# Performance work log

Measured on AMD Instinct MI355X. Metric: run time of the kernel, lower is better.

## Reference

```python
import jax, jax.numpy as jnp
import numpy as np

NEG_SLOPE = 0.15
MASK_VAL = -1e9


def setup_inputs() -> dict:
    key = jax.random.key(0)
    k1, k2, k3, k4, k5 = jax.random.split(key, 5)
    B, N, D, H, QKV = 4, 1024, 128, 8, 16
    h = jax.random.normal(k1, (B, N, D), dtype=jnp.float32)
    same_cluster = jax.random.randint(k2, (B, N, N), 0, 2) > 0
    # nn.Linear weights stored as [in, out] (x @ W); scaled like default init
    Wa = jax.random.normal(k3, (2 * D + 1, H), dtype=jnp.float32) / np.sqrt(2 * D + 1)
    Wv = jax.random.normal(k4, (D, H * QKV), dtype=jnp.float32) / np.sqrt(D)
    Wo = jax.random.normal(k5, (H * QKV, D), dtype=jnp.float32) / np.sqrt(H * QKV)
    return {"h": h, "same_cluster": same_cluster, "Wa": Wa, "Wv": Wv, "Wo": Wo, "local_only": 0}


def reference(h, same_cluster, Wa, Wv, Wo, local_only):
    B, N, D = h.shape
    H = Wa.shape[1]
    # concat([hi, hj, edge]) @ Wa == hi @ Wa[:D] + hj @ Wa[D:2D] + edge * Wa[2D]
    Wa_i, Wa_j, w_e = Wa[:D], Wa[D:2 * D], Wa[2 * D]  # [D,H], [D,H], [H]
    s_i = h @ Wa_i  # [B, N, H]
    s_j = h @ Wa_j  # [B, N, H]
    edge = same_cluster.astype(h.dtype)  # [B, N, N]
    scores = s_i[:, :, None, :] + s_j[:, None, :, :] + edge[..., None] * w_e  # [B,N,N,H]
    scores = jax.nn.leaky_relu(scores, negative_slope=NEG_SLOPE)
    scores = jnp.moveaxis(scores, -1, 1)  # [B, H, N, N]
    if local_only:
        scores = jnp.where(same_cluster[:, None, :, :], scores, MASK_VAL)
    alpha = jax.nn.softmax(scores, axis=-1)  # [B, H, N, N]
    v = (h @ Wv).reshape(B, N, H, -1).transpose(0, 2, 1, 3)  # [B, H, N, qkv]
    out = jnp.einsum('bhij,bhjd->bhid', alpha, v)  # [B, H, N, qkv]
    out = out.transpose(0, 2, 1, 3).reshape(B, N, -1)  # [B, N, H*qkv]
    return out @ Wo  # [B, N, D]
```

## Files before the change

### kernel.cpp

```cpp
#include <hip/hip_runtime.h>
#include <hip/hip_fp16.h>


#define NEG_SLOPE 0.15f
#define LOG2E 1.442695040888963f
#define B_ 4
#define N_ 1024
#define D_ 128
#define H_ 8
#define QKV_ 16
#define BN_ (B_ * N_)

typedef _Float16 half8 __attribute__((ext_vector_type(8)));
typedef float f32x4 __attribute__((ext_vector_type(4)));

#define WS_BYTES ((size_t)3932160)

__global__ __launch_bounds__(256) void prep_kernel(
    const float* __restrict__ h, const int* __restrict__ edge,
    const float* __restrict__ Wa, const float* __restrict__ Wv,
    float* __restrict__ SIt, float* __restrict__ SJt,
    _Float16* __restrict__ VT, unsigned long long* __restrict__ EM)
{
    __shared__ float hl[8][128];
    const int t  = threadIdx.x;
    const int w  = t >> 6;
    const int l  = t & 63;
    const int R0 = blockIdx.x * 8;

    {
        const int f = t * 4;
        *(float4*)(&hl[0][0] + f) = *(const float4*)(h + (size_t)R0 * 128 + f);
    }
    __syncthreads();

    const int cq = t & 31, rq = t >> 5;
    const int c4 = cq * 4;
    float a0 = 0.f, a1 = 0.f, a2 = 0.f, a3 = 0.f;
    #pragma unroll 8
    for (int k = 0; k < 128; ++k) {
        const float4 wv = *(const float4*)(Wv + k * 128 + c4);
        const float a = hl[rq][k];
        a0 += a * wv.x; a1 += a * wv.y; a2 += a * wv.z; a3 += a * wv.w;
    }
    {
        const int R = R0 + rq, b = R >> 10, n = R & 1023;
        const int head = cq >> 2, dd = (cq & 3) * 4;
        _Float16* vt = VT + ((size_t)(b * H_ + head) * 16 + dd) * N_ + n;
        vt[0]      = (_Float16)a0;
        vt[N_]     = (_Float16)a1;
        vt[2 * N_] = (_Float16)a2;
        vt[3 * N_] = (_Float16)a3;
    }

    {
        const int task = t >> 1, half = t & 1;
        const int row = task >> 4, which = (task >> 3) & 1, hh = task & 7;
        const float* wcol = Wa + which * 128 * H_ + hh;
        float s = 0.f;
        #pragma unroll 8
        for (int kk = 0; kk < 64; ++kk) {
            const int k = half * 64 + kk;
            s += hl[row][k] * wcol[k * H_];
        }
        s += __shfl_xor(s, 1, 64);
        if (!half) (which ? SJt : SIt)[hh * BN_ + R0 + row] = s * LOG2E;
    }

    #pragma unroll
    for (int rr = 0; rr < 2; ++rr) {
        const int R = R0 + w * 2 + rr;
        const int* erow = edge + (size_t)R * N_;
        #pragma unroll 4
        for (int s = 0; s < 16; ++s) {
            const unsigned long long mk = __ballot(erow[s * 64 + l] != 0);
            if (l == 0) EM[(size_t)R * 16 + s] = mk;
        }
    }
}

__global__ __launch_bounds__(256) void attn_kernel(
    const float* __restrict__ SIt, const float* __restrict__ SJt,
    const _Float16* __restrict__ VT, const unsigned long long* __restrict__ EM,
    const float* __restrict__ Wa, const int* __restrict__ local_only,
    float* __restrict__ ATT)
{
    const int t  = threadIdx.x;
    const int w  = t >> 6;
    const int l  = t & 63;
    const int m  = l & 15;
    const int kq = l >> 4;
    const int hh = blockIdx.y;
    const int b  = blockIdx.z;
    const int i0 = blockIdx.x * 16;
    const int bn0 = b * N_;

    const float we = Wa[2 * D_ * H_ + hh] * LOG2E;
    const int   lo = local_only[0];

    const float sim   = SIt[hh * BN_ + bn0 + i0 + m];
    const float simwe = sim + we;
    const float simNE = lo ? -1e6f : sim;

    const float*         sjrow = SJt + hh * BN_ + bn0;
    const _Float16*      vrow  = VT + ((size_t)(b * H_ + hh) * 16 + m) * N_;
    const unsigned char* EMb   = (const unsigned char*)EM;
    const size_t         eb0   = (size_t)(bn0 + i0 + m) * 128 + w * 32 + kq;

    f32x4 acc = {0.f, 0.f, 0.f, 0.f};
    float dsum = 0.f;

    const int wj0 = w * 256;
    #pragma unroll 2
    for (int c = 0; c < 8; ++c) {
        const int jb = wj0 + c * 32 + kq * 8;
        const float4 sjA = *(const float4*)(sjrow + jb);
        const float4 sjB = *(const float4*)(sjrow + jb + 4);
        const half8  bf  = *(const half8*)(vrow + jb);
        const int    eb  = EMb[eb0 + c * 4];

        const float sj[8] = {sjA.x, sjA.y, sjA.z, sjA.w,
                             sjB.x, sjB.y, sjB.z, sjB.w};
        half8 av;
        #pragma unroll
        for (int u = 0; u < 8; ++u) {
            const float x  = (((eb >> u) & 1) ? simwe : simNE) + sj[u];
            const float sc = fmaxf(x, NEG_SLOPE * x);
            const float p  = exp2f(sc);
            dsum += p;
            av[u] = (_Float16)p;
        }
        acc = __builtin_amdgcn_mfma_f32_16x16x32_f16(av, bf, acc, 0, 0, 0);
    }

    dsum += __shfl_xor(dsum, 16, 64);
    dsum += __shfl_xor(dsum, 32, 64);

    __shared__ float olds[4][16][17];
    __shared__ float denl[4][16];
    #pragma unroll
    for (int reg = 0; reg < 4; ++reg)
        olds[w][kq * 4 + reg][m] = acc[reg];
    if (l < 16) denl[w][l] = dsum;
    __syncthreads();

    {
        const int i = t >> 4, d = t & 15;
        const float o   = olds[0][i][d] + olds[1][i][d]
                        + olds[2][i][d] + olds[3][i][d];
        const float den = denl[0][i] + denl[1][i] + denl[2][i] + denl[3][i];
        ATT[(size_t)(bn0 + i0 + i) * 128 + hh * 16 + d] = o / den;
    }
}

__global__ __launch_bounds__(256) void out_kernel(
    const float* __restrict__ ATT, const float* __restrict__ Wo,
    float* __restrict__ out)
{
    __shared__ float al[8][128];
    const int t  = threadIdx.x;
    const int R0 = blockIdx.x * 8;
    {
        const int f = t * 4;
        *(float4*)(&al[0][0] + f) = *(const float4*)(ATT + (size_t)R0 * 128 + f);
    }
    __syncthreads();

    const int cq = t & 31, rq = t >> 5;
    const int c4 = cq * 4;
    float a0 = 0.f, a1 = 0.f, a2 = 0.f, a3 = 0.f;
    #pragma unroll 8
    for (int k = 0; k < 128; ++k) {
        const float4 wv = *(const float4*)(Wo + k * 128 + c4);
        const float a = al[rq][k];
        a0 += a * wv.x; a1 += a * wv.y; a2 += a * wv.z; a3 += a * wv.w;
    }
    float4 o; o.x = a0; o.y = a1; o.z = a2; o.w = a3;
    *(float4*)(out + (size_t)(R0 + rq) * 128 + c4) = o;
}

extern "C" void kernel_launch(void* const* d_in, const int* in_sizes, int n_in,
                              void* d_out, int out_size, void* d_ws, size_t ws_size,
                              hipStream_t stream) {
    const float* h    = (const float*)d_in[0];
    const int*   edge = (const int*)d_in[1];
    const float* Wa   = (const float*)d_in[2];
    const float* Wv   = (const float*)d_in[3];
    const float* Wo   = (const float*)d_in[4];
    const int*   lo   = (const int*)d_in[5];
    float*       out  = (float*)d_out;

    hipMemsetAsync(d_ws, 0, WS_BYTES, stream);

    char* ws = (char*)d_ws;
    float*              SIt = (float*)(ws);
    float*              SJt = (float*)(ws + 131072);
    float*              ATT = (float*)(ws + 262144);
    _Float16*           VT  = (_Float16*)(ws + 2359296);
    unsigned long long* EM  = (unsigned long long*)(ws + 3407872);

    prep_kernel<<<BN_ / 8, 256, 0, stream>>>(h, edge, Wa, Wv, SIt, SJt, VT, EM);
    attn_kernel<<<dim3(N_ / 16, H_, B_), 256, 0, stream>>>(SIt, SJt, VT, EM, Wa, lo, ATT);
    out_kernel<<<BN_ / 8, 256, 0, stream>>>(ATT, Wo, out);
}
```

Baseline: 130.6 us.

## Fuse prep, attention and output kernels into one cooperative persistent kernel

Merges the three kernels into one cooperative launch of 512 blocks, separated by grid-wide syncs, and each block loops over four attention tiles. The aim is to remove two kernel launch gaps and the tail effects between stages. In exchange it pays for grid.sync barriers and limits occupancy to the cooperative grid size. The memset is still issued.

```diff
diff --git a/kernel.cpp b/kernel.cpp
--- a/kernel.cpp
+++ b/kernel.cpp
@@ -1,5 +1,8 @@
 #include <hip/hip_runtime.h>
+#include <hip/hip_cooperative_groups.h>
 #include <hip/hip_fp16.h>
+
+namespace cg = cooperative_groups;
 
 
 #define NEG_SLOPE 0.15f
@@ -10,173 +13,167 @@
 #define H_ 8
 #define QKV_ 16
 #define BN_ (B_ * N_)
+#define GRID_ 512
 
 typedef _Float16 half8 __attribute__((ext_vector_type(8)));
 typedef float f32x4 __attribute__((ext_vector_type(4)));
 
 #define WS_BYTES ((size_t)3932160)
 
-__global__ __launch_bounds__(256) void prep_kernel(
+__global__ __launch_bounds__(256, 2) void fused_kernel(
     const float* __restrict__ h, const int* __restrict__ edge,
     const float* __restrict__ Wa, const float* __restrict__ Wv,
+    const float* __restrict__ Wo, const int* __restrict__ local_only,
     float* __restrict__ SIt, float* __restrict__ SJt,
-    _Float16* __restrict__ VT, unsigned long long* __restrict__ EM)
+    float* __restrict__ ATT, _Float16* __restrict__ VT,
+    unsigned long long* __restrict__ EM, float* __restrict__ out)
 {
+    cg::grid_group grid = cg::this_grid();
     __shared__ float hl[8][128];
-    const int t  = threadIdx.x;
-    const int w  = t >> 6;
-    const int l  = t & 63;
-    const int R0 = blockIdx.x * 8;
+    __shared__ float olds[4][16][17];
+    __shared__ float denl[4][16];
+
+    const int t   = threadIdx.x;
+    const int bid = blockIdx.x;
+    const int w   = t >> 6;
+    const int l   = t & 63;
 
     {
-        const int f = t * 4;
-        *(float4*)(&hl[0][0] + f) = *(const float4*)(h + (size_t)R0 * 128 + f);
+        const int R0 = bid * 8;
+        {
+            const int f = t * 4;
+            *(float4*)(&hl[0][0] + f) = *(const float4*)(h + (size_t)R0 * 128 + f);
+        }
+        __syncthreads();
+
+        const int cq = t & 31, rq = t >> 5;
+        const int c4 = cq * 4;
+        float a0 = 0.f, a1 = 0.f, a2 = 0.f, a3 = 0.f;
+        #pragma unroll 8
+        for (int k = 0; k < 128; ++k) {
+            const float4 wv = *(const float4*)(Wv + k * 128 + c4);
+            const float a = hl[rq][k];
+            a0 += a * wv.x; a1 += a * wv.y; a2 += a * wv.z; a3 += a * wv.w;
+        }
+        {
+            const int R = R0 + rq, b = R >> 10, n = R & 1023;
+            const int head = cq >> 2, dd = (cq & 3) * 4;
+            _Float16* vt = VT + ((size_t)(b * H_ + head) * 16 + dd) * N_ + n;
+            vt[0]      = (_Float16)a0;
+            vt[N_]     = (_Float16)a1;
+            vt[2 * N_] = (_Float16)a2;
+            vt[3 * N_] = (_Float16)a3;
+        }
+
+        {
+            const int task = t >> 1, half = t & 1;
+            const int row = task >> 4, which = (task >> 3) & 1, hh = task & 7;
+            const float* wcol = Wa + which * 128 * H_ + hh;
+            float s = 0.f;
+            #pragma unroll 8
+            for (int kk = 0; kk < 64; ++kk) {
+                const int k = half * 64 + kk;
+                s += hl[row][k] * wcol[k * H_];
+            }
+            s += __shfl_xor(s, 1, 64);
+            if (!half) (which ? SJt : SIt)[hh * BN_ + R0 + row] = s * LOG2E;
+        }
+
+        #pragma unroll
+        for (int rr = 0; rr < 2; ++rr) {
+            const int R = R0 + w * 2 + rr;
+            const int* erow = edge + (size_t)R * N_;
+            #pragma unroll 4
+            for (int s = 0; s < 16; ++s) {
+                const unsigned long long mk = __ballot(erow[s * 64 + l] != 0);
+                if (l == 0) EM[(size_t)R * 16 + s] = mk;
+            }
+        }
     }
-    __syncthreads();
-
-    const int cq = t & 31, rq = t >> 5;
-    const int c4 = cq * 4;
-    float a0 = 0.f, a1 = 0.f, a2 = 0.f, a3 = 0.f;
-    #pragma unroll 8
-    for (int k = 0; k < 128; ++k) {
-        const float4 wv = *(const float4*)(Wv + k * 128 + c4);
-        const float a = hl[rq][k];
-        a0 += a * wv.x; a1 += a * wv.y; a2 += a * wv.z; a3 += a * wv.w;
-    }
-    {
-        const int R = R0 + rq, b = R >> 10, n = R & 1023;
-        const int head = cq >> 2, dd = (cq & 3) * 4;
-        _Float16* vt = VT + ((size_t)(b * H_ + head) * 16 + dd) * N_ + n;
-        vt[0]      = (_Float16)a0;
-        vt[N_]     = (_Float16)a1;
-        vt[2 * N_] = (_Float16)a2;
-        vt[3 * N_] = (_Float16)a3;
-    }
-
-    {
-        const int task = t >> 1, half = t & 1;
-        const int row = task >> 4, which = (task >> 3) & 1, hh = task & 7;
-        const float* wcol = Wa + which * 128 * H_ + hh;
-        float s = 0.f;
-        #pragma unroll 8
-        for (int kk = 0; kk < 64; ++kk) {
-            const int k = half * 64 + kk;
-            s += hl[row][k] * wcol[k * H_];
-        }
-        s += __shfl_xor(s, 1, 64);
-        if (!half) (which ? SJt : SIt)[hh * BN_ + R0 + row] = s * LOG2E;
-    }
-
-    #pragma unroll
-    for (int rr = 0; rr < 2; ++rr) {
-        const int R = R0 + w * 2 + rr;
-        const int* erow = edge + (size_t)R * N_;
-        #pragma unroll 4
-        for (int s = 0; s < 16; ++s) {
-            const unsigned long long mk = __ballot(erow[s * 64 + l] != 0);
-            if (l == 0) EM[(size_t)R * 16 + s] = mk;
-        }
-    }
-}
-
-__global__ __launch_bounds__(256) void attn_kernel(
-    const float* __restrict__ SIt, const float* __restrict__ SJt,
-    const _Float16* __restrict__ VT, const unsigned long long* __restrict__ EM,
-    const float* __restrict__ Wa, const int* __restrict__ local_only,
-    float* __restrict__ ATT)
-{
-    const int t  = threadIdx.x;
-    const int w  = t >> 6;
-    const int l  = t & 63;
+
+    grid.sync();
+
+    const int lo = local_only[0];
+    const unsigned char* EMb = (const unsigned char*)EM;
     const int m  = l & 15;
     const int kq = l >> 4;
-    const int hh = blockIdx.y;
-    const int b  = blockIdx.z;
-    const int i0 = blockIdx.x * 16;
-    const int bn0 = b * N_;
-
-    const float we = Wa[2 * D_ * H_ + hh] * LOG2E;
-    const int   lo = local_only[0];
-
-    const float sim   = SIt[hh * BN_ + bn0 + i0 + m];
-    const float simwe = sim + we;
-    const float simNE = lo ? -1e6f : sim;
-
-    const float*         sjrow = SJt + hh * BN_ + bn0;
-    const _Float16*      vrow  = VT + ((size_t)(b * H_ + hh) * 16 + m) * N_;
-    const unsigned char* EMb   = (const unsigned char*)EM;
-    const size_t         eb0   = (size_t)(bn0 + i0 + m) * 128 + w * 32 + kq;
-
-    f32x4 acc = {0.f, 0.f, 0.f, 0.f};
-    float dsum = 0.f;
-
-    const int wj0 = w * 256;
-    #pragma unroll 2
-    for (int c = 0; c < 8; ++c) {
-        const int jb = wj0 + c * 32 + kq * 8;
-        const float4 sjA = *(const float4*)(sjrow + jb);
-        const float4 sjB = *(const float4*)(sjrow + jb + 4);
-        const half8  bf  = *(const half8*)(vrow + jb);
-        const int    eb  = EMb[eb0 + c * 4];
-
-        const float sj[8] = {sjA.x, sjA.y, sjA.z, sjA.w,
-                             sjB.x, sjB.y, sjB.z, sjB.w};
-        half8 av;
+    for (int q = 0; q < 4; ++q) {
+        const int tile = bid + GRID_ * q;
+        const int b   = tile >> 9;
+        const int hh  = (tile >> 6) & 7;
+        const int i0  = (tile & 63) * 16;
+        const int bn0 = b * N_;
+
+        const float we    = Wa[2 * D_ * H_ + hh] * LOG2E;
+        const float sim   = SIt[hh * BN_ + bn0 + i0 + m];
+        const float simwe = sim + we;
+        const float simNE = lo ? -1e6f : sim;
+        const float*    sjrow = SJt + hh * BN_ + bn0;
+        const _Float16* vrow  = VT + ((size_t)(b * H_ + hh) * 16 + m) * N_;
+        const size_t    eb0   = (size_t)(bn0 + i0 + m) * 128 + w * 32 + kq;
+
+        f32x4 acc = {0.f, 0.f, 0.f, 0.f};
+        float dsum = 0.f;
+        const int wj0 = w * 256;
+        #pragma unroll 2
+        for (int c = 0; c < 8; ++c) {
+            const int jb = wj0 + c * 32 + kq * 8;
+            const float4 sjA = *(const float4*)(sjrow + jb);
+            const float4 sjB = *(const float4*)(sjrow + jb + 4);
+            const half8  bf  = *(const half8*)(vrow + jb);
+            const int    eb  = EMb[eb0 + c * 4];
+            const float sj[8] = {sjA.x, sjA.y, sjA.z, sjA.w,
+                                 sjB.x, sjB.y, sjB.z, sjB.w};
+            half8 av;
+            #pragma unroll
+            for (int u = 0; u < 8; ++u) {
+                const float x  = (((eb >> u) & 1) ? simwe : simNE) + sj[u];
+                const float sc = fmaxf(x, NEG_SLOPE * x);
+                const float p  = exp2f(sc);
+                dsum += p;
+                av[u] = (_Float16)p;
+            }
+            acc = __builtin_amdgcn_mfma_f32_16x16x32_f16(av, bf, acc, 0, 0, 0);
+        }
+        dsum += __shfl_xor(dsum, 16, 64);
+        dsum += __shfl_xor(dsum, 32, 64);
+
         #pragma unroll
-        for (int u = 0; u < 8; ++u) {
-            const float x  = (((eb >> u) & 1) ? simwe : simNE) + sj[u];
-            const float sc = fmaxf(x, NEG_SLOPE * x);
-            const float p  = exp2f(sc);
-            dsum += p;
-            av[u] = (_Float16)p;
-        }
-        acc = __builtin_amdgcn_mfma_f32_16x16x32_f16(av, bf, acc, 0, 0, 0);
+        for (int reg = 0; reg < 4; ++reg)
+            olds[w][kq * 4 + reg][m] = acc[reg];
+        if (l < 16) denl[w][l] = dsum;
+        __syncthreads();
+        {
+            const int i = t >> 4, d = t & 15;
+            const float o   = olds[0][i][d] + olds[1][i][d]
+                            + olds[2][i][d] + olds[3][i][d];
+            const float den = denl[0][i] + denl[1][i] + denl[2][i] + denl[3][i];
+            ATT[(size_t)(bn0 + i0 + i) * 128 + hh * 16 + d] = o / den;
+        }
+        __syncthreads();
     }
 
-    dsum += __shfl_xor(dsum, 16, 64);
-    dsum += __shfl_xor(dsum, 32, 64);
-
-    __shared__ float olds[4][16][17];
-    __shared__ float denl[4][16];
-    #pragma unroll
-    for (int reg = 0; reg < 4; ++reg)
-        olds[w][kq * 4 + reg][m] = acc[reg];
-    if (l < 16) denl[w][l] = dsum;
-    __syncthreads();
+    grid.sync();
 
     {
-        const int i = t >> 4, d = t & 15;
-        const float o   = olds[0][i][d] + olds[1][i][d]
-                        + olds[2][i][d] + olds[3][i][d];
-        const float den = denl[0][i] + denl[1][i] + denl[2][i] + denl[3][i];
-        ATT[(size_t)(bn0 + i0 + i) * 128 + hh * 16 + d] = o / den;
+        const int R0 = bid * 8;
+        {
+            const int f = t * 4;
+            *(float4*)(&hl[0][0] + f) = *(const float4*)(ATT + (size_t)R0 * 128 + f);
+        }
+        __syncthreads();
+        const int cq = t & 31, rq = t >> 5;
+        const int c4 = cq * 4;
+        float a0 = 0.f, a1 = 0.f, a2 = 0.f, a3 = 0.f;
+        #pragma unroll 8
+        for (int k = 0; k < 128; ++k) {
+            const float4 wv = *(const float4*)(Wo + k * 128 + c4);
+            const float a = hl[rq][k];
+            a0 += a * wv.x; a1 += a * wv.y; a2 += a * wv.z; a3 += a * wv.w;
+        }
+        float4 o; o.x = a0; o.y = a1; o.z = a2; o.w = a3;
+        *(float4*)(out + (size_t)(R0 + rq) * 128 + c4) = o;
     }
-}
-
-__global__ __launch_bounds__(256) void out_kernel(
-    const float* __restrict__ ATT, const float* __restrict__ Wo,
-    float* __restrict__ out)
-{
-    __shared__ float al[8][128];
-    const int t  = threadIdx.x;
-    const int R0 = blockIdx.x * 8;
-    {
-        const int f = t * 4;
-        *(float4*)(&al[0][0] + f) = *(const float4*)(ATT + (size_t)R0 * 128 + f);
-    }
-    __syncthreads();
-
-    const int cq = t & 31, rq = t >> 5;
-    const int c4 = cq * 4;
-    float a0 = 0.f, a1 = 0.f, a2 = 0.f, a3 = 0.f;
-    #pragma unroll 8
-    for (int k = 0; k < 128; ++k) {
-        const float4 wv = *(const float4*)(Wo + k * 128 + c4);
-        const float a = al[rq][k];
-        a0 += a * wv.x; a1 += a * wv.y; a2 += a * wv.z; a3 += a * wv.w;
-    }
-    float4 o; o.x = a0; o.y = a1; o.z = a2; o.w = a3;
-    *(float4*)(out + (size_t)(R0 + rq) * 128 + c4) = o;
 }
 
 extern "C" void kernel_launch(void* const* d_in, const int* in_sizes, int n_in,
@@ -199,7 +196,9 @@
     _Float16*           VT  = (_Float16*)(ws + 2359296);
     unsigned long long* EM  = (unsigned long long*)(ws + 3407872);
 
-    prep_kernel<<<BN_ / 8, 256, 0, stream>>>(h, edge, Wa, Wv, SIt, SJt, VT, EM);
-    attn_kernel<<<dim3(N_ / 16, H_, B_), 256, 0, stream>>>(SIt, SJt, VT, EM, Wa, lo, ATT);
-    out_kernel<<<BN_ / 8, 256, 0, stream>>>(ATT, Wo, out);
+    void* args[] = { (void*)&h, (void*)&edge, (void*)&Wa, (void*)&Wv,
+                     (void*)&Wo, (void*)&lo, (void*)&SIt, (void*)&SJt,
+                     (void*)&ATT, (void*)&VT, (void*)&EM, (void*)&out };
+    hipLaunchCooperativeKernel((void*)fused_kernel, dim3(GRID_), dim3(256),
+                               args, 0, stream);
 }
```

Result: slower. 243.2 us (+86.1%).
